# Kernel tuning notes

Hardware: AMD Instinct MI355X
Metric: run time of the kernel (lower is better)

The kernel has to match this reference:

```python
import jax, jax.numpy as jnp
import numpy as np

N_USERS = 100000
N_ITEMS = 200000
N_NODES = N_USERS + N_ITEMS
EMB_DIM = 64
N_EDGES = 4000000
N_LAYERS = 2
BATCH = 8192
EMB_REG = 2.5e-5


def setup_inputs() -> dict:
    key = jax.random.key(0)
    k = jax.random.split(key, 7)
    return {
        "user_emb": jax.random.normal(k[0], (N_USERS, EMB_DIM), jnp.float32) * 0.1,
        "item_emb": jax.random.normal(k[1], (N_ITEMS, EMB_DIM), jnp.float32) * 0.1,
        "all_h": jax.random.randint(k[2], (N_EDGES,), 0, N_NODES, jnp.int64 if jax.config.jax_enable_x64 else jnp.int32),
        "all_t": jax.random.randint(k[3], (N_EDGES,), 0, N_NODES, jnp.int64 if jax.config.jax_enable_x64 else jnp.int32),
        "users": jax.random.randint(k[4], (BATCH,), 0, N_USERS),
        "pos_items": jax.random.randint(k[5], (BATCH,), 0, N_ITEMS),
        "neg_items": jax.random.randint(k[6], (BATCH,), 0, N_ITEMS),
    }


def _spmm(h, t, vals, x):
    # out[h] += vals * x[t]  over all edges; [N_NODES, D]
    return jax.ops.segment_sum(vals[:, None] * x[t], h, num_segments=N_NODES)


def reference(user_emb, item_emb, all_h, all_t, users, pos_items, neg_items):
    # symmetric normalization G = D^{-1/2} A D^{-1/2} on the edge list
    deg = jax.ops.segment_sum(jnp.ones((all_h.shape[0],), user_emb.dtype), all_h,
                              num_segments=N_NODES)
    dinv = jnp.where(deg > 0, deg ** -0.5, 0.0)
    g_vals = dinv[all_h] * dinv[all_t]

    # inference1: n_layers of SpMM with residual; sum over all layer outputs
    # (dropout p=0 on the main branch in the source -> identity)
    emb = jnp.concatenate([user_emb, item_emb], axis=0)  # [N, D]
    acc = emb
    for _ in range(N_LAYERS):
        emb = _spmm(all_h, all_t, g_vals, emb) + emb
        acc = acc + emb
    ua, ia = acc[:N_USERS], acc[N_USERS:]

    # BPR loss on the batch
    u = ua[users]
    pos = ia[pos_items]
    neg = ia[neg_items]
    pos_scores = jnp.sum(u * pos, axis=1)
    neg_scores = jnp.sum(u * neg, axis=1)
    mf_loss = jnp.mean(jax.nn.softplus(neg_scores - pos_scores))

    # embedding L2 regularization on the pre-propagation embeddings
    u_pre = user_emb[users]
    pos_pre = item_emb[pos_items]
    neg_pre = item_emb[neg_items]
    emb_loss = EMB_REG * (jnp.sum(u_pre ** 2) + jnp.sum(pos_pre ** 2)
                          + jnp.sum(neg_pre ** 2))
    return (mf_loss, emb_loss)
```

## Files before the change

kernel.cpp:

```cpp
#include <hip/hip_runtime.h>
#include <math.h>

#define N_USERS 100000
#define N_ITEMS 200000
#define N_NODES 300000
#define EMB_DIM 64
#define N_EDGES 4000000
#define BATCH   8192
#define EMB_REG 2.5e-05f

#define BUCK_SH 9
#define BN      512
#define NBUCK   586
#define BSLOT   7424
#define EPB     8192
#define EPT     32
#define NBLK_A  489
#define PACK_SH 19
#define SCORE_BLOCKS (BATCH / 4)

typedef unsigned short u16;
typedef unsigned int   u32;
typedef unsigned char  u8;
typedef __attribute__((ext_vector_type(8))) u16 u16x8;
typedef __attribute__((ext_vector_type(2))) float f32x2;

__device__ __forceinline__ float bf2f(u16 x) {
    u32 u = ((u32)x) << 16;
    return __builtin_bit_cast(float, u);
}
__device__ __forceinline__ u16 f2bf(float f) {
    u32 u = __builtin_bit_cast(u32, f);
    return (u16)((u + 0x7FFFu + ((u >> 16) & 1u)) >> 16);
}

__global__ void k_init(int* __restrict__ bcur) {
    int i = blockIdx.x * blockDim.x + threadIdx.x;
    if (i < NBUCK) bcur[i] = i * BSLOT;
}

__global__ void k_mark(const int* __restrict__ users, const int* __restrict__ pos,
                       const int* __restrict__ neg, u8* __restrict__ flags) {
    int i = blockIdx.x * blockDim.x + threadIdx.x;
    if (i < BATCH) {
        flags[users[i]] = 1;
        flags[N_USERS + pos[i]] = 1;
        flags[N_USERS + neg[i]] = 1;
    }
}

__global__ __launch_bounds__(256) void kA(const int* __restrict__ hh,
                                          const int* __restrict__ tt,
                                          int* __restrict__ bcur, int* __restrict__ gp) {
    __shared__ int sh_cnt[NBUCK];
    __shared__ int sh_base[NBUCK];
    int tid = threadIdx.x;
    for (int j = tid; j < NBUCK; j += 256) sh_cnt[j] = 0;
    __syncthreads();
    int cbase = blockIdx.x * EPB;
    int clen  = min(EPB, N_EDGES - cbase);
    int pk[EPT], bk[EPT];
    #pragma unroll
    for (int j = 0; j < EPT; ++j) {
        int i = j * 256 + tid;
        bk[j] = -1;
        if (i < clen) {
            int h = hh[cbase + i];
            int t = tt[cbase + i];
            int b = h >> BUCK_SH;
            bk[j] = b;
            pk[j] = ((h & (BN - 1)) << PACK_SH) | t;
            atomicAdd(&sh_cnt[b], 1);
        }
    }
    __syncthreads();
    for (int j = tid; j < NBUCK; j += 256) {
        int c = sh_cnt[j];
        sh_base[j] = c ? atomicAdd(&bcur[j], c) : 0;
        sh_cnt[j] = 0;
    }
    __syncthreads();
    #pragma unroll
    for (int j = 0; j < EPT; ++j) {
        if (bk[j] >= 0) {
            int r = atomicAdd(&sh_cnt[bk[j]], 1);
            gp[sh_base[bk[j]] + r] = pk[j];
        }
    }
}

__global__ __launch_bounds__(256) void kB(const int* __restrict__ bcur,
                                          int* __restrict__ gp,
                                          int2* __restrict__ sde, float* __restrict__ dinv,
                                          const float* __restrict__ uemb,
                                          const float* __restrict__ iemb,
                                          u8* __restrict__ e0s8) {
    __shared__ int   ncnt[BN];
    __shared__ int   noff[BN];
    __shared__ float sdv[BN];
    __shared__ int   slots[BSLOT];
    int b = blockIdx.x;
    int node0 = b << BUCK_SH;
    int nn = min(BN, N_NODES - node0);
    int base = b * BSLOT;
    int count = bcur[b] - base;
    int tid = threadIdx.x;
    for (int j = tid; j < BN; j += 256) ncnt[j] = 0;
    __syncthreads();
    for (int i = tid; i < count; i += 256)
        atomicAdd(&ncnt[gp[base + i] >> PACK_SH], 1);
    __syncthreads();
    if (tid < 64) {
        int lane = tid, carry = 0;
        #pragma unroll
        for (int b0 = 0; b0 < BN; b0 += 64) {
            int idx = b0 + lane;
            int v = ncnt[idx];
            int incl = v;
            #pragma unroll
            for (int d = 1; d < 64; d <<= 1) {
                int u = __shfl_up(incl, d, 64);
                if (lane >= d) incl += u;
            }
            noff[idx] = carry + incl - v;
            carry += __shfl(incl, 63, 64);
        }
    }
    __syncthreads();
    for (int j = tid; j < nn; j += 256) {
        int c = ncnt[j];
        float dv = c > 0 ? rsqrtf((float)c) : 0.0f;
        sde[node0 + j]  = make_int2(base + noff[j], c);
        dinv[node0 + j] = dv;
        sdv[j] = dv;
    }
    __syncthreads();
    for (int j = tid; j < BN; j += 256) ncnt[j] = noff[j];
    __syncthreads();
    for (int i = tid; i < count; i += 256) {
        int p = gp[base + i];
        int r = atomicAdd(&ncnt[p >> PACK_SH], 1);
        slots[r] = p & ((1 << PACK_SH) - 1);
    }
    __syncthreads();
    for (int i = tid; i < count; i += 256)
        gp[base + i] = slots[i];
    for (int i = tid; i < nn * 8; i += 256) {
        int j = i >> 3;
        float sc = sdv[j];
        int gnode = node0 + j;
        size_t ebase = (size_t)gnode * EMB_DIM + (size_t)(i & 7) * 8;
        const size_t UELEMS = (size_t)N_USERS * EMB_DIM;
        const float* src = (ebase < UELEMS) ? uemb + ebase : iemb + (ebase - UELEMS);
        float4 a  = ((const float4*)src)[0];
        float4 c4 = ((const float4*)src)[1];
        u32 w0 = __builtin_amdgcn_cvt_pk_fp8_f32(sc * a.x,  sc * a.y,  0,  false);
        w0 = __builtin_amdgcn_cvt_pk_fp8_f32(sc * a.z,  sc * a.w,  w0, true);
        u32 w1 = __builtin_amdgcn_cvt_pk_fp8_f32(sc * c4.x, sc * c4.y, 0,  false);
        w1 = __builtin_amdgcn_cvt_pk_fp8_f32(sc * c4.z, sc * c4.w, w1, true);
        uint2 o; o.x = w0; o.y = w1;
        ((uint2*)e0s8)[(size_t)gnode * 8 + (i & 7)] = o;
    }
}

__global__ __launch_bounds__(256) void k_spmm1(const int2* __restrict__ sde,
                        const int* __restrict__ et,
                        const u8* __restrict__ src8,
                        const float* __restrict__ uemb, const float* __restrict__ iemb,
                        const u8* __restrict__ flags,
                        u16* __restrict__ dstb, u8* __restrict__ dst8) {
    int lane = threadIdx.x & 63;
    int g    = lane >> 3;
    int sl   = lane & 7;
    int gb   = lane & 56;
    int node = blockIdx.x * 32 + ((threadIdx.x >> 6) << 3) + g;
    int2 se = sde[node];
    int s = se.x, ne = se.y;
    float dh = ne > 0 ? rsqrtf((float)ne) : 0.0f;
    int mx = ne;
    mx = max(mx, __shfl_xor(mx, 8, 64));
    mx = max(mx, __shfl_xor(mx, 16, 64));
    mx = max(mx, __shfl_xor(mx, 32, 64));
    float acc[8] = {0.f, 0.f, 0.f, 0.f, 0.f, 0.f, 0.f, 0.f};
    for (int j0 = 0; j0 < mx; j0 += 8) {
        int idx = j0 + sl;
        int ets = (idx < ne) ? et[s + idx] : 0;
        #pragma unroll
        for (int jj = 0; jj < 8; ++jj) {
            if (j0 + jj < ne) {
                int t = __shfl(ets, gb | jj, 64);
                uint2 d8 = ((const uint2*)(src8 + (size_t)t * EMB_DIM))[sl];
                f32x2 p0 = __builtin_amdgcn_cvt_pk_f32_fp8(d8.x, false);
                f32x2 p1 = __builtin_amdgcn_cvt_pk_f32_fp8(d8.x, true);
                f32x2 p2 = __builtin_amdgcn_cvt_pk_f32_fp8(d8.y, false);
                f32x2 p3 = __builtin_amdgcn_cvt_pk_f32_fp8(d8.y, true);
                acc[0] += p0.x; acc[1] += p0.y;
                acc[2] += p1.x; acc[3] += p1.y;
                acc[4] += p2.x; acc[5] += p2.y;
                acc[6] += p3.x; acc[7] += p3.y;
            }
        }
    }
    const float* srow = (node < N_USERS)
        ? uemb + (size_t)node * EMB_DIM
        : iemb + (size_t)(node - N_USERS) * EMB_DIM;
    float4 a = ((const float4*)srow)[sl * 2];
    float4 c = ((const float4*)srow)[sl * 2 + 1];
    float v[8];
    v[0] = dh * acc[0] + a.x; v[1] = dh * acc[1] + a.y;
    v[2] = dh * acc[2] + a.z; v[3] = dh * acc[3] + a.w;
    v[4] = dh * acc[4] + c.x; v[5] = dh * acc[5] + c.y;
    v[6] = dh * acc[6] + c.z; v[7] = dh * acc[7] + c.w;
    u32 w0 = __builtin_amdgcn_cvt_pk_fp8_f32(dh * v[0], dh * v[1], 0, false);
    w0 = __builtin_amdgcn_cvt_pk_fp8_f32(dh * v[2], dh * v[3], w0, true);
    u32 w1 = __builtin_amdgcn_cvt_pk_fp8_f32(dh * v[4], dh * v[5], 0, false);
    w1 = __builtin_amdgcn_cvt_pk_fp8_f32(dh * v[6], dh * v[7], w1, true);
    uint2 ow; ow.x = w0; ow.y = w1;
    ((uint2*)(dst8 + (size_t)node * EMB_DIM))[sl] = ow;
    if (flags[node]) {
        u16x8 o;
        o.s0 = f2bf(v[0]); o.s1 = f2bf(v[1]); o.s2 = f2bf(v[2]); o.s3 = f2bf(v[3]);
        o.s4 = f2bf(v[4]); o.s5 = f2bf(v[5]); o.s6 = f2bf(v[6]); o.s7 = f2bf(v[7]);
        ((u16x8*)(dstb + (size_t)node * EMB_DIM))[sl] = o;
    }
}

__global__ void k_score(const int* __restrict__ users, const int* __restrict__ pos,
                        const int* __restrict__ neg,
                        const float* __restrict__ uemb, const float* __restrict__ iemb,
                        const u16* __restrict__ emb1b, const u8* __restrict__ emb1s8,
                        const int2* __restrict__ sde, const int* __restrict__ et,
                        const float* __restrict__ dinv,
                        float* __restrict__ pmf, float* __restrict__ psq) {
    __shared__ float smf[4], ssq[4];
    int gid = blockIdx.x * blockDim.x + threadIdx.x;
    int b = gid >> 6;
    int d = gid & 63;
    int w = threadIdx.x >> 6;
    int u  = users[b];
    int pi = pos[b];
    int ni = neg[b];
    int nodes[3];
    nodes[0] = u; nodes[1] = N_USERS + pi; nodes[2] = N_USERS + ni;
    float pre[3];
    pre[0] = uemb[(size_t)u * EMB_DIM + d];
    pre[1] = iemb[(size_t)pi * EMB_DIM + d];
    pre[2] = iemb[(size_t)ni * EMB_DIM + d];
    int s0[3], ne[3], ets[3];
    float dv[3];
    #pragma unroll
    for (int k = 0; k < 3; ++k) {
        int v = nodes[k];
        int2 se = sde[v];
        s0[k] = se.x; ne[k] = se.y;
        dv[k] = dinv[v];
        ets[k] = (d < ne[k]) ? et[se.x + d] : 0;
    }
    float a[3];
    #pragma unroll
    for (int k = 0; k < 3; ++k) {
        float ac = 0.f;
        int lim = ne[k] < 64 ? ne[k] : 64;
        for (int j = 0; j < lim; ++j) {
            int t = __shfl(ets[k], j, 64);
            u32 byte = emb1s8[(size_t)t * EMB_DIM + d];
            ac += __builtin_amdgcn_cvt_f32_fp8(byte, 0);
        }
        for (int i = s0[k] + 64; i < s0[k] + ne[k]; ++i) {
            int t = et[i];
            u32 byte = emb1s8[(size_t)t * EMB_DIM + d];
            ac += __builtin_amdgcn_cvt_f32_fp8(byte, 0);
        }
        a[k] = pre[k] + 2.0f * bf2f(emb1b[(size_t)nodes[k] * EMB_DIM + d]) + dv[k] * ac;
    }
    float ps = a[0] * a[1];
    float ns = a[0] * a[2];
    float sq = pre[0] * pre[0] + pre[1] * pre[1] + pre[2] * pre[2];
    #pragma unroll
    for (int off2 = 32; off2 > 0; off2 >>= 1) {
        ps += __shfl_down(ps, off2, 64);
        ns += __shfl_down(ns, off2, 64);
        sq += __shfl_down(sq, off2, 64);
    }
    if (d == 0) {
        float x  = ns - ps;
        smf[w] = fmaxf(x, 0.0f) + log1pf(expf(-fabsf(x)));
        ssq[w] = sq;
    }
    __syncthreads();
    if (threadIdx.x == 0) {
        pmf[blockIdx.x] = smf[0] + smf[1] + smf[2] + smf[3];
        psq[blockIdx.x] = ssq[0] + ssq[1] + ssq[2] + ssq[3];
    }
}

__global__ void k_final(const float* __restrict__ pmf, const float* __restrict__ psq,
                        float* __restrict__ out) {
    __shared__ float smf[4], ssq[4];
    int tid = threadIdx.x;
    float mf = 0.f, sq = 0.f;
    #pragma unroll
    for (int i = 0; i < SCORE_BLOCKS / 256; ++i) {
        mf += pmf[tid + i * 256];
        sq += psq[tid + i * 256];
    }
    #pragma unroll
    for (int off2 = 32; off2 > 0; off2 >>= 1) {
        mf += __shfl_down(mf, off2, 64);
        sq += __shfl_down(sq, off2, 64);
    }
    if ((tid & 63) == 0) { smf[tid >> 6] = mf; ssq[tid >> 6] = sq; }
    __syncthreads();
    if (tid == 0) {
        out[0] = (smf[0] + smf[1] + smf[2] + smf[3]) * (1.0f / BATCH);
        out[1] = EMB_REG * (ssq[0] + ssq[1] + ssq[2] + ssq[3]);
    }
}

extern "C" void kernel_launch(void* const* d_in, const int* in_sizes, int n_in,
                              void* d_out, int out_size, void* d_ws, size_t ws_size,
                              hipStream_t stream) {
    const float* uemb  = (const float*)d_in[0];
    const float* iemb  = (const float*)d_in[1];
    const int*   all_h = (const int*)d_in[2];
    const int*   all_t = (const int*)d_in[3];
    const int*   users = (const int*)d_in[4];
    const int*   pos   = (const int*)d_in[5];
    const int*   neg   = (const int*)d_in[6];
    float* out = (float*)d_out;

    int*   ws     = (int*)d_ws;
    float* dinv   = (float*)ws;
    int2*  sde    = (int2*)(ws + 300032);
    int*   bcur   = ws + 900096;
    u8*    flags  = (u8*)(ws + 901120);
    float* pmf    = (float*)(ws + 976128);
    float* psq    = (float*)(ws + 978176);
    int*   gp     = ws + 980224;
    u8*    e0s8   = (u8*)(ws + 5330688);
    u8*    emb1s8 = (u8*)(ws + 10130688);
    u16*   emb1b  = (u16*)(ws + 14930688);

    hipMemsetAsync(flags, 0, N_NODES, stream);

    k_init <<<3, 256, 0, stream>>>(bcur);
    k_mark <<<BATCH / 256, 256, 0, stream>>>(users, pos, neg, flags);
    kA     <<<NBLK_A, 256, 0, stream>>>(all_h, all_t, bcur, gp);
    kB     <<<NBUCK, 256, 0, stream>>>(bcur, gp, sde, dinv, uemb, iemb, e0s8);

    k_spmm1<<<N_NODES / 32, 256, 0, stream>>>(sde, gp, e0s8, uemb, iemb,
                                              flags, emb1b, emb1s8);

    k_score<<<SCORE_BLOCKS, 256, 0, stream>>>(users, pos, neg, uemb, iemb,
                                              emb1b, emb1s8, sde, gp, dinv, pmf, psq);
    k_final<<<1, 256, 0, stream>>>(pmf, psq, out);
}
```

Measured before the change: 304.0 us.

## Fuse init/mark into bucketing kernel, stage scatter in LDS, widen SpMM gathers

Removes the k_init and k_mark launches. Flag marking moves into extra blocks of kA, and bucket cursors are zeroed by one larger memset that now covers both flags and bcur. kA sorts each chunk by bucket in shared memory with a prefix scan and then writes gp in bucket-contiguous runs, aiming for more coalesced global stores. The SpMM now uses 4 lanes per node with 16-byte fp8 loads and a zeroed sentinel row for padded edges, which drops per-edge branching and per-group max-degree loops. The cost is more shared memory in kA, which may lower occupancy, and wasted sentinel loads on padded edges.

```diff
diff --git a/kernel.cpp b/kernel.cpp
--- a/kernel.cpp
+++ b/kernel.cpp
@@ -16,6 +16,7 @@
 #define EPB     8192
 #define EPT     32
 #define NBLK_A  489
+#define NBLK_MARK (BATCH / 256)
 #define PACK_SH 19
 #define SCORE_BLOCKS (BATCH / 4)
 
@@ -34,26 +35,30 @@
     return (u16)((u + 0x7FFFu + ((u >> 16) & 1u)) >> 16);
 }
 
-__global__ void k_init(int* __restrict__ bcur) {
-    int i = blockIdx.x * blockDim.x + threadIdx.x;
-    if (i < NBUCK) bcur[i] = i * BSLOT;
-}
-
-__global__ void k_mark(const int* __restrict__ users, const int* __restrict__ pos,
-                       const int* __restrict__ neg, u8* __restrict__ flags) {
-    int i = blockIdx.x * blockDim.x + threadIdx.x;
-    if (i < BATCH) {
-        flags[users[i]] = 1;
-        flags[N_USERS + pos[i]] = 1;
-        flags[N_USERS + neg[i]] = 1;
-    }
-}
-
 __global__ __launch_bounds__(256) void kA(const int* __restrict__ hh,
                                           const int* __restrict__ tt,
-                                          int* __restrict__ bcur, int* __restrict__ gp) {
+                                          int* __restrict__ bcur, int* __restrict__ gp,
+                                          const int* __restrict__ users,
+                                          const int* __restrict__ pos,
+                                          const int* __restrict__ neg,
+                                          u8* __restrict__ flags,
+                                          u8* __restrict__ e0s8) {
+    if (blockIdx.x >= NBLK_A) {
+        int i = (blockIdx.x - NBLK_A) * 256 + threadIdx.x;
+        if (i < BATCH) {
+            flags[users[i]] = 1;
+            flags[N_USERS + pos[i]] = 1;
+            flags[N_USERS + neg[i]] = 1;
+        }
+        if (blockIdx.x == NBLK_A && threadIdx.x < 16)
+            ((int*)(e0s8 + (size_t)N_NODES * EMB_DIM))[threadIdx.x] = 0;
+        return;
+    }
     __shared__ int sh_cnt[NBUCK];
+    __shared__ int sh_off[NBUCK];
     __shared__ int sh_base[NBUCK];
+    __shared__ int stage[EPB];
+    __shared__ u16 sbid[EPB];
     int tid = threadIdx.x;
     for (int j = tid; j < NBUCK; j += 256) sh_cnt[j] = 0;
     __syncthreads();
@@ -74,9 +79,25 @@
         }
     }
     __syncthreads();
+    if (tid < 64) {
+        int lane = tid, carry = 0;
+        for (int b0 = 0; b0 < NBUCK; b0 += 64) {
+            int idx = b0 + lane;
+            int v = (idx < NBUCK) ? sh_cnt[idx] : 0;
+            int incl = v;
+            #pragma unroll
+            for (int d = 1; d < 64; d <<= 1) {
+                int u = __shfl_up(incl, d, 64);
+                if (lane >= d) incl += u;
+            }
+            if (idx < NBUCK) sh_off[idx] = carry + incl - v;
+            carry += __shfl(incl, 63, 64);
+        }
+    }
+    __syncthreads();
     for (int j = tid; j < NBUCK; j += 256) {
         int c = sh_cnt[j];
-        sh_base[j] = c ? atomicAdd(&bcur[j], c) : 0;
+        sh_base[j] = j * BSLOT + (c ? atomicAdd(&bcur[j], c) : 0);
         sh_cnt[j] = 0;
     }
     __syncthreads();
@@ -84,8 +105,15 @@
     for (int j = 0; j < EPT; ++j) {
         if (bk[j] >= 0) {
             int r = atomicAdd(&sh_cnt[bk[j]], 1);
-            gp[sh_base[bk[j]] + r] = pk[j];
-        }
+            int p = sh_off[bk[j]] + r;
+            stage[p] = pk[j];
+            sbid[p]  = (u16)bk[j];
+        }
+    }
+    __syncthreads();
+    for (int i = tid; i < clen; i += 256) {
+        int b = sbid[i];
+        gp[sh_base[b] + i - sh_off[b]] = stage[i];
     }
 }
 
@@ -103,7 +131,7 @@
     int node0 = b << BUCK_SH;
     int nn = min(BN, N_NODES - node0);
     int base = b * BSLOT;
-    int count = bcur[b] - base;
+    int count = bcur[b];
     int tid = threadIdx.x;
     for (int j = tid; j < BN; j += 256) ncnt[j] = 0;
     __syncthreads();
@@ -170,58 +198,72 @@
                         const u8* __restrict__ flags,
                         u16* __restrict__ dstb, u8* __restrict__ dst8) {
     int lane = threadIdx.x & 63;
-    int g    = lane >> 3;
-    int sl   = lane & 7;
-    int gb   = lane & 56;
-    int node = blockIdx.x * 32 + ((threadIdx.x >> 6) << 3) + g;
-    int2 se = sde[node];
+    int g    = lane >> 2;
+    int sl   = lane & 3;
+    int gb   = lane & 60;
+    int node = blockIdx.x * 64 + ((threadIdx.x >> 6) << 4) + g;
+    bool alive = node < N_NODES;
+    int2 se = alive ? sde[node] : make_int2(0, 0);
     int s = se.x, ne = se.y;
     float dh = ne > 0 ? rsqrtf((float)ne) : 0.0f;
-    int mx = ne;
-    mx = max(mx, __shfl_xor(mx, 8, 64));
-    mx = max(mx, __shfl_xor(mx, 16, 64));
-    mx = max(mx, __shfl_xor(mx, 32, 64));
-    float acc[8] = {0.f, 0.f, 0.f, 0.f, 0.f, 0.f, 0.f, 0.f};
-    for (int j0 = 0; j0 < mx; j0 += 8) {
+    float acc[16];
+    #pragma unroll
+    for (int k = 0; k < 16; ++k) acc[k] = 0.f;
+    int nb = (ne + 3) & ~3;
+    for (int j0 = 0; j0 < nb; j0 += 4) {
         int idx = j0 + sl;
-        int ets = (idx < ne) ? et[s + idx] : 0;
+        int ets = (idx < ne) ? et[s + idx] : N_NODES;
         #pragma unroll
-        for (int jj = 0; jj < 8; ++jj) {
-            if (j0 + jj < ne) {
-                int t = __shfl(ets, gb | jj, 64);
-                uint2 d8 = ((const uint2*)(src8 + (size_t)t * EMB_DIM))[sl];
-                f32x2 p0 = __builtin_amdgcn_cvt_pk_f32_fp8(d8.x, false);
-                f32x2 p1 = __builtin_amdgcn_cvt_pk_f32_fp8(d8.x, true);
-                f32x2 p2 = __builtin_amdgcn_cvt_pk_f32_fp8(d8.y, false);
-                f32x2 p3 = __builtin_amdgcn_cvt_pk_f32_fp8(d8.y, true);
-                acc[0] += p0.x; acc[1] += p0.y;
-                acc[2] += p1.x; acc[3] += p1.y;
-                acc[4] += p2.x; acc[5] += p2.y;
-                acc[6] += p3.x; acc[7] += p3.y;
-            }
-        }
-    }
+        for (int jj = 0; jj < 4; ++jj) {
+            int t = __shfl(ets, gb | jj, 64);
+            uint4 d8 = ((const uint4*)(src8 + (size_t)t * EMB_DIM))[sl];
+            f32x2 p;
+            p = __builtin_amdgcn_cvt_pk_f32_fp8(d8.x, false); acc[0]  += p.x; acc[1]  += p.y;
+            p = __builtin_amdgcn_cvt_pk_f32_fp8(d8.x, true);  acc[2]  += p.x; acc[3]  += p.y;
+            p = __builtin_amdgcn_cvt_pk_f32_fp8(d8.y, false); acc[4]  += p.x; acc[5]  += p.y;
+            p = __builtin_amdgcn_cvt_pk_f32_fp8(d8.y, true);  acc[6]  += p.x; acc[7]  += p.y;
+            p = __builtin_amdgcn_cvt_pk_f32_fp8(d8.z, false); acc[8]  += p.x; acc[9]  += p.y;
+            p = __builtin_amdgcn_cvt_pk_f32_fp8(d8.z, true);  acc[10] += p.x; acc[11] += p.y;
+            p = __builtin_amdgcn_cvt_pk_f32_fp8(d8.w, false); acc[12] += p.x; acc[13] += p.y;
+            p = __builtin_amdgcn_cvt_pk_f32_fp8(d8.w, true);  acc[14] += p.x; acc[15] += p.y;
+        }
+    }
+    if (!alive) return;
     const float* srow = (node < N_USERS)
         ? uemb + (size_t)node * EMB_DIM
         : iemb + (size_t)(node - N_USERS) * EMB_DIM;
-    float4 a = ((const float4*)srow)[sl * 2];
-    float4 c = ((const float4*)srow)[sl * 2 + 1];
-    float v[8];
-    v[0] = dh * acc[0] + a.x; v[1] = dh * acc[1] + a.y;
-    v[2] = dh * acc[2] + a.z; v[3] = dh * acc[3] + a.w;
-    v[4] = dh * acc[4] + c.x; v[5] = dh * acc[5] + c.y;
-    v[6] = dh * acc[6] + c.z; v[7] = dh * acc[7] + c.w;
-    u32 w0 = __builtin_amdgcn_cvt_pk_fp8_f32(dh * v[0], dh * v[1], 0, false);
-    w0 = __builtin_amdgcn_cvt_pk_fp8_f32(dh * v[2], dh * v[3], w0, true);
-    u32 w1 = __builtin_amdgcn_cvt_pk_fp8_f32(dh * v[4], dh * v[5], 0, false);
-    w1 = __builtin_amdgcn_cvt_pk_fp8_f32(dh * v[6], dh * v[7], w1, true);
-    uint2 ow; ow.x = w0; ow.y = w1;
-    ((uint2*)(dst8 + (size_t)node * EMB_DIM))[sl] = ow;
+    float4 a0 = ((const float4*)srow)[sl * 4 + 0];
+    float4 a1 = ((const float4*)srow)[sl * 4 + 1];
+    float4 a2 = ((const float4*)srow)[sl * 4 + 2];
+    float4 a3 = ((const float4*)srow)[sl * 4 + 3];
+    float v[16];
+    v[0]  = dh * acc[0]  + a0.x; v[1]  = dh * acc[1]  + a0.y;
+    v[2]  = dh * acc[2]  + a0.z; v[3]  = dh * acc[3]  + a0.w;
+    v[4]  = dh * acc[4]  + a1.x; v[5]  = dh * acc[5]  + a1.y;
+    v[6]  = dh * acc[6]  + a1.z; v[7]  = dh * acc[7]  + a1.w;
+    v[8]  = dh * acc[8]  + a2.x; v[9]  = dh * acc[9]  + a2.y;
+    v[10] = dh * acc[10] + a2.z; v[11] = dh * acc[11] + a2.w;
+    v[12] = dh * acc[12] + a3.x; v[13] = dh * acc[13] + a3.y;
+    v[14] = dh * acc[14] + a3.z; v[15] = dh * acc[15] + a3.w;
+    uint4 ow;
+    u32 w;
+    w = __builtin_amdgcn_cvt_pk_fp8_f32(dh * v[0],  dh * v[1],  0, false);
+    w = __builtin_amdgcn_cvt_pk_fp8_f32(dh * v[2],  dh * v[3],  w, true);  ow.x = w;
+    w = __builtin_amdgcn_cvt_pk_fp8_f32(dh * v[4],  dh * v[5],  0, false);
+    w = __builtin_amdgcn_cvt_pk_fp8_f32(dh * v[6],  dh * v[7],  w, true);  ow.y = w;
+    w = __builtin_amdgcn_cvt_pk_fp8_f32(dh * v[8],  dh * v[9],  0, false);
+    w = __builtin_amdgcn_cvt_pk_fp8_f32(dh * v[10], dh * v[11], w, true);  ow.z = w;
+    w = __builtin_amdgcn_cvt_pk_fp8_f32(dh * v[12], dh * v[13], 0, false);
+    w = __builtin_amdgcn_cvt_pk_fp8_f32(dh * v[14], dh * v[15], w, true);  ow.w = w;
+    ((uint4*)(dst8 + (size_t)node * EMB_DIM))[sl] = ow;
     if (flags[node]) {
-        u16x8 o;
-        o.s0 = f2bf(v[0]); o.s1 = f2bf(v[1]); o.s2 = f2bf(v[2]); o.s3 = f2bf(v[3]);
-        o.s4 = f2bf(v[4]); o.s5 = f2bf(v[5]); o.s6 = f2bf(v[6]); o.s7 = f2bf(v[7]);
-        ((u16x8*)(dstb + (size_t)node * EMB_DIM))[sl] = o;
+        u16x8 o0, o1;
+        o0.s0 = f2bf(v[0]);  o0.s1 = f2bf(v[1]);  o0.s2 = f2bf(v[2]);  o0.s3 = f2bf(v[3]);
+        o0.s4 = f2bf(v[4]);  o0.s5 = f2bf(v[5]);  o0.s6 = f2bf(v[6]);  o0.s7 = f2bf(v[7]);
+        o1.s0 = f2bf(v[8]);  o1.s1 = f2bf(v[9]);  o1.s2 = f2bf(v[10]); o1.s3 = f2bf(v[11]);
+        o1.s4 = f2bf(v[12]); o1.s5 = f2bf(v[13]); o1.s6 = f2bf(v[14]); o1.s7 = f2bf(v[15]);
+        ((u16x8*)(dstb + (size_t)node * EMB_DIM))[sl * 2]     = o0;
+        ((u16x8*)(dstb + (size_t)node * EMB_DIM))[sl * 2 + 1] = o1;
     }
 }
 
@@ -332,24 +374,23 @@
     int*   ws     = (int*)d_ws;
     float* dinv   = (float*)ws;
     int2*  sde    = (int2*)(ws + 300032);
-    int*   bcur   = ws + 900096;
-    u8*    flags  = (u8*)(ws + 901120);
+    u8*    flags  = (u8*)(ws + 900096);
+    int*   bcur   = ws + 975104;
     float* pmf    = (float*)(ws + 976128);
     float* psq    = (float*)(ws + 978176);
     int*   gp     = ws + 980224;
     u8*    e0s8   = (u8*)(ws + 5330688);
-    u8*    emb1s8 = (u8*)(ws + 10130688);
-    u16*   emb1b  = (u16*)(ws + 14930688);
-
-    hipMemsetAsync(flags, 0, N_NODES, stream);
-
-    k_init <<<3, 256, 0, stream>>>(bcur);
-    k_mark <<<BATCH / 256, 256, 0, stream>>>(users, pos, neg, flags);
-    kA     <<<NBLK_A, 256, 0, stream>>>(all_h, all_t, bcur, gp);
-    kB     <<<NBUCK, 256, 0, stream>>>(bcur, gp, sde, dinv, uemb, iemb, e0s8);
-
-    k_spmm1<<<N_NODES / 32, 256, 0, stream>>>(sde, gp, e0s8, uemb, iemb,
-                                              flags, emb1b, emb1s8);
+    u8*    emb1s8 = (u8*)(ws + 10130944);
+    u16*   emb1b  = (u16*)(ws + 14930944);
+
+    hipMemsetAsync(flags, 0, 304128, stream);
+
+    kA <<<NBLK_A + NBLK_MARK, 256, 0, stream>>>(all_h, all_t, bcur, gp,
+                                                users, pos, neg, flags, e0s8);
+    kB <<<NBUCK, 256, 0, stream>>>(bcur, gp, sde, dinv, uemb, iemb, e0s8);
+
+    k_spmm1<<<(N_NODES + 63) / 64, 256, 0, stream>>>(sde, gp, e0s8, uemb, iemb,
+                                                     flags, emb1b, emb1s8);
 
     k_score<<<SCORE_BLOCKS, 256, 0, stream>>>(users, pos, neg, uemb, iemb,
                                               emb1b, emb1s8, sde, gp, dinv, pmf, psq);
```

Result: faster. 289.6 us (-4.7%).
